# Performance work log

Hardware: AMD Instinct MI355X
Metric: run time of the kernel (lower is better)

## Reference

```python
import jax, jax.numpy as jnp
import numpy as np
import math

NUM_HEADS = 8

def setup_inputs() -> dict:
    key = jax.random.key(0)
    ks = jax.random.split(key, 5)
    b, h, w, c = 4, 128, 128, 256
    x = jax.random.normal(ks[0], (b, h, w, c), dtype=jnp.float32)
    scale = 1.0 / math.sqrt(c)  # keep weights reasonably scaled (kaiming-like)
    Wq = jax.random.normal(ks[1], (c, c), dtype=jnp.float32) * scale
    Wk = jax.random.normal(ks[2], (c, c), dtype=jnp.float32) * scale
    Wv = jax.random.normal(ks[3], (c, c), dtype=jnp.float32) * scale
    Wout = jax.random.normal(ks[4], (c, c), dtype=jnp.float32) * scale
    return {"x": x, "Wq": Wq, "Wk": Wk, "Wv": Wv, "Wout": Wout}

def reference(x, Wq, Wk, Wv, Wout):
    b, h, w, c = x.shape
    hw = h * w
    heads = NUM_HEADS
    dh = c // heads
    xs = x.reshape(b, hw, c)
    q = xs @ Wq  # (b, hw, c)
    k = xs @ Wk
    v = xs @ Wv

    def split_heads(t):
        # (b, hw, c) -> (b, c, hw) -> (b, heads, dh, hw)
        return t.transpose(0, 2, 1).reshape(b, heads, dh, hw)

    q = split_heads(q)
    k = split_heads(k)
    v = split_heads(v)
    # L2-normalize along the feature (hw) axis; original has no epsilon
    q = q / jnp.linalg.norm(q, axis=-1, keepdims=True)
    k = k / jnp.linalg.norm(k, axis=-1, keepdims=True)
    d_k = q.shape[-1]  # = hw
    attn = jnp.einsum('bhcd,bhed->bhce', q, k) / math.sqrt(d_k)  # (b,heads,dh,dh)
    attn = jax.nn.softmax(attn, axis=-1)
    vals = jnp.einsum('bhce,bhed->bhcd', attn, v)  # (b,heads,dh,hw)
    vals = vals.transpose(0, 3, 1, 2).reshape(b, hw, c)
    out = (vals @ Wout).reshape(b, h, w, c)
    return out
```

## Files before the change

### kernel.cpp

```cpp
#include <hip/hip_runtime.h>


#define B_   4
#define HW_  16384
#define C_   256

typedef __attribute__((ext_vector_type(8))) short short8;
typedef __attribute__((ext_vector_type(4))) float floatx4;

__device__ __forceinline__ unsigned short f2bf(float f) {
  unsigned u = __builtin_bit_cast(unsigned, f);
  u += 0x7FFFu + ((u >> 16) & 1u);
  return (unsigned short)(u >> 16);
}

__device__ __forceinline__ void gl_lds16(const unsigned short* g, unsigned short* l) {
  __builtin_amdgcn_global_load_lds(
      (const __attribute__((address_space(1))) unsigned int*)g,
      (__attribute__((address_space(3))) unsigned int*)l, 16, 0, 0);
}

__global__ __launch_bounds__(256) void k_cast_tr(const float* __restrict__ x,
                                                 unsigned short* __restrict__ xb,
                                                 unsigned short* __restrict__ xT,
                                                 float* __restrict__ S) {
  __shared__ unsigned short lds[64][72];
  int bid = blockIdx.x;
  int t = threadIdx.x;
  if (bid < 256) {
    float4 z = {0.f, 0.f, 0.f, 0.f};
    ((float4*)S)[bid * 256 + t] = z;
  }
  int ct = bid & 3;
  int pt = (bid >> 2) & 255;
  int b  = bid >> 10;
  const float* src = x + ((size_t)(b * HW_ + pt * 64)) * C_ + ct * 64;
#pragma unroll
  for (int e = 0; e < 4; e++) {
    int lin = t + e * 256;
    int p = lin >> 4, c4 = lin & 15;
    float4 v = *(const float4*)(src + (size_t)p * C_ + c4 * 4);
    ushort4 h;
    h.x = f2bf(v.x); h.y = f2bf(v.y); h.z = f2bf(v.z); h.w = f2bf(v.w);
    *(ushort4*)(xb + ((size_t)(b * HW_ + pt * 64 + p)) * C_ + ct * 64 + c4 * 4) = h;
    lds[c4 * 4 + 0][p] = h.x;
    lds[c4 * 4 + 1][p] = h.y;
    lds[c4 * 4 + 2][p] = h.z;
    lds[c4 * 4 + 3][p] = h.w;
  }
  __syncthreads();
#pragma unroll
  for (int e = 0; e < 4; e++) {
    int lin = t + e * 256;
    int c = lin >> 4, p4 = lin & 15;
    ushort4 h;
    h.x = lds[c][p4 * 4 + 0];
    h.y = lds[c][p4 * 4 + 1];
    h.z = lds[c][p4 * 4 + 2];
    h.w = lds[c][p4 * 4 + 3];
    *(ushort4*)(xT + ((size_t)(b * C_ + ct * 64 + c)) * HW_ + pt * 64 + p4 * 4) = h;
  }
}

template <int NST>
__device__ __forceinline__ void nt_loop(const unsigned short* Ab, int lda,
                                        const unsigned short* Bb, int ldb,
                                        unsigned short* At, unsigned short* Bt,
                                        floatx4 acc[4][4]) {
  int t = threadIdx.x;
  int lane = t & 63, w = t >> 6;
  int wm = w >> 1, wn = w & 1;
  int l8 = lane >> 3, l7 = lane & 7;
  int srcoct = l7 ^ l8;
  int l15 = lane & 15, l4 = lane >> 4;
  for (int s = 0; s < NST; s++) {
#pragma unroll
    for (int i = 0; i < 4; i++) {
      int gi = w * 4 + i;
      int row = gi * 8 + l8;
      gl_lds16(Ab + (size_t)row * lda + s * 64 + srcoct * 8, At + gi * 512);
      gl_lds16(Bb + (size_t)row * ldb + s * 64 + srcoct * 8, Bt + gi * 512);
    }
    __syncthreads();
#pragma unroll
    for (int kk = 0; kk < 2; kk++) {
      short8 af[4], bfv[4];
#pragma unroll
      for (int tm = 0; tm < 4; tm++) {
        int row = wm * 64 + tm * 16 + l15;
        int oct = kk * 4 + l4;
        af[tm] = *(const short8*)(At + row * 64 + ((oct ^ (l15 & 7)) * 8));
      }
#pragma unroll
      for (int tn = 0; tn < 4; tn++) {
        int row = wn * 64 + tn * 16 + l15;
        int oct = kk * 4 + l4;
        bfv[tn] = *(const short8*)(Bt + row * 64 + ((oct ^ (l15 & 7)) * 8));
      }
#pragma unroll
      for (int tm = 0; tm < 4; tm++)
#pragma unroll
        for (int tn = 0; tn < 4; tn++)
          acc[tm][tn] = __builtin_amdgcn_mfma_f32_16x16x32_bf16(af[tm], bfv[tn],
                                                                acc[tm][tn], 0, 0, 0);
    }
    __syncthreads();
  }
}

__global__ __launch_bounds__(256) void k_sgemm(const unsigned short* __restrict__ xT,
                                               float* __restrict__ S) {
  __shared__ unsigned short At[128 * 64];
  __shared__ unsigned short Bt[128 * 64];
  int bid = blockIdx.x;
  int ks = bid & 31, nt = (bid >> 5) & 1, mt = (bid >> 6) & 1, b = bid >> 7;
  const unsigned short* Ab = xT + ((size_t)(b * C_ + mt * 128)) * HW_ + ks * 512;
  const unsigned short* Bb = xT + ((size_t)(b * C_ + nt * 128)) * HW_ + ks * 512;
  floatx4 acc[4][4];
  floatx4 z = {0.f, 0.f, 0.f, 0.f};
#pragma unroll
  for (int i = 0; i < 4; i++)
#pragma unroll
    for (int j = 0; j < 4; j++) acc[i][j] = z;
  nt_loop<8>(Ab, HW_, Bb, HW_, At, Bt, acc);
  int t = threadIdx.x, lane = t & 63, w = t >> 6;
  int wm = w >> 1, wn = w & 1;
  int l15 = lane & 15, l4 = lane >> 4;
  float* Sb = S + (size_t)b * 65536;
#pragma unroll
  for (int tm = 0; tm < 4; tm++)
#pragma unroll
    for (int tn = 0; tn < 4; tn++)
#pragma unroll
      for (int r = 0; r < 4; r++) {
        int m = mt * 128 + wm * 64 + tm * 16 + l4 * 4 + r;
        int n = nt * 128 + wn * 64 + tn * 16 + l15;
        atomicAdd(Sb + (size_t)m * C_ + n, acc[tm][tn][r]);
      }
}

__global__ __launch_bounds__(256) void k_gemm_sw(const float* __restrict__ S,
                                                 const float* __restrict__ Wq,
                                                 const float* __restrict__ Wk,
                                                 float* __restrict__ SWq,
                                                 float* __restrict__ SWk) {
  __shared__ float As[64][17];
  __shared__ float Bs[16][65];
  int bid = blockIdx.x;
  int nt = bid & 7, mt = (bid >> 3) & 3, b = bid >> 5;
  int mb = mt * 64;
  const float* Wsel = (nt < 4) ? Wq : Wk;
  int nb = (nt & 3) * 64;
  int t = threadIdx.x, tx = t & 15, ty = t >> 4;
  float acc[4][4] = {};
  for (int kt = 0; kt < 16; kt++) {
    {
      int row = t >> 2, kq = t & 3;
      float4 v = *(const float4*)(S + ((size_t)(b * C_ + mb + row)) * C_ + kt * 16 + kq * 4);
      As[row][kq * 4 + 0] = v.x; As[row][kq * 4 + 1] = v.y;
      As[row][kq * 4 + 2] = v.z; As[row][kq * 4 + 3] = v.w;
    }
    {
      int kk = t >> 4, n4 = t & 15;
      float4 v = *(const float4*)(Wsel + ((size_t)(kt * 16 + kk)) * C_ + nb + n4 * 4);
      Bs[kk][n4 * 4 + 0] = v.x; Bs[kk][n4 * 4 + 1] = v.y;
      Bs[kk][n4 * 4 + 2] = v.z; Bs[kk][n4 * 4 + 3] = v.w;
    }
    __syncthreads();
#pragma unroll
    for (int k = 0; k < 16; k++) {
      float a[4], bb[4];
#pragma unroll
      for (int i = 0; i < 4; i++) a[i] = As[ty * 4 + i][k];
#pragma unroll
      for (int j = 0; j < 4; j++) bb[j] = Bs[k][tx * 4 + j];
#pragma unroll
      for (int i = 0; i < 4; i++)
#pragma unroll
        for (int j = 0; j < 4; j++) acc[i][j] += a[i] * bb[j];
    }
    __syncthreads();
  }
#pragma unroll
  for (int i = 0; i < 4; i++)
#pragma unroll
    for (int j = 0; j < 4; j++) {
      int row = mb + ty * 4 + i;
      int ng = nt * 64 + tx * 4 + j;
      if (ng < 256) SWq[((size_t)(b * C_ + row)) * C_ + ng] = acc[i][j];
      else          SWk[((size_t)(b * C_ + row)) * C_ + ng - 256] = acc[i][j];
    }
}

__global__ __launch_bounds__(256) void k_fuse(const float* __restrict__ Wq,
                                              const float* __restrict__ Wk,
                                              const float* __restrict__ SWq,
                                              const float* __restrict__ SWk,
                                              const float* __restrict__ Wout,
                                              float* __restrict__ U) {
  __shared__ float Wqh[256][32];
  __shared__ float Wkh[256][32];
  __shared__ float SWqh[256][32];
  __shared__ float SWkh[256][32];
  __shared__ float Lg[32][33];
  __shared__ float qp[8][32], kp[8][32], qin[32], kin[32];
  int b = blockIdx.x >> 3, h = blockIdx.x & 7;
  int t = threadIdx.x;
  int col = t & 31, rgrp = t >> 5;
  for (int r0 = 0; r0 < 256; r0 += 8) {
    int row = r0 + rgrp;
    Wqh[row][col]  = Wq[(size_t)row * C_ + h * 32 + col];
    Wkh[row][col]  = Wk[(size_t)row * C_ + h * 32 + col];
    SWqh[row][col] = SWq[((size_t)(b * C_ + row)) * C_ + h * 32 + col];
    SWkh[row][col] = SWk[((size_t)(b * C_ + row)) * C_ + h * 32 + col];
  }
  __syncthreads();
  {
    float g[4] = {0.f, 0.f, 0.f, 0.f};
    for (int k = 0; k < 256; k++) {
      float swk = SWkh[k][col];
#pragma unroll
      for (int r = 0; r < 4; r++) g[r] += Wqh[k][rgrp + 8 * r] * swk;
    }
#pragma unroll
    for (int r = 0; r < 4; r++) Lg[rgrp + 8 * r][col] = g[r];
  }
  {
    float sq = 0.f, sk = 0.f;
    for (int k = rgrp * 32; k < rgrp * 32 + 32; k++) {
      sq += Wqh[k][col] * SWqh[k][col];
      sk += Wkh[k][col] * SWkh[k][col];
    }
    qp[rgrp][col] = sq;
    kp[rgrp][col] = sk;
  }
  __syncthreads();
  if (t < 32) {
    float a = 0.f;
#pragma unroll
    for (int p = 0; p < 8; p++) a += qp[p][t];
    qin[t] = rsqrtf(a);
  } else if (t < 64) {
    int j = t - 32;
    float a = 0.f;
#pragma unroll
    for (int p = 0; p < 8; p++) a += kp[p][j];
    kin[j] = rsqrtf(a);
  }
  __syncthreads();
  if (t < 32) {
    float row[32];
    float mx = -1e30f;
#pragma unroll
    for (int j = 0; j < 32; j++) {
      row[j] = Lg[t][j] * qin[t] * kin[j] * 0.0078125f;
      mx = fmaxf(mx, row[j]);
    }
    float sum = 0.f;
#pragma unroll
    for (int j = 0; j < 32; j++) { row[j] = __expf(row[j] - mx); sum += row[j]; }
    float inv = 1.0f / sum;
#pragma unroll
    for (int j = 0; j < 32; j++) Lg[t][j] = row[j] * inv;
  }
  __syncthreads();
  float (*Wo)[256] = reinterpret_cast<float(*)[256]>(&Wqh[0][0]);
#pragma unroll
  for (int r = 0; r < 32; r++) Wo[r][t] = Wout[((size_t)(h * 32 + r)) * C_ + t];
  __syncthreads();
  for (int j = 0; j < 32; j++) {
    float a = 0.f;
#pragma unroll
    for (int i2 = 0; i2 < 32; i2++) a += Lg[i2][j] * Wo[i2][t];
    U[((size_t)(b * C_ + h * 32 + j)) * C_ + t] = a;
  }
}

__global__ __launch_bounds__(256) void k_gemm_w3(const float* __restrict__ Wv,
                                                 const float* __restrict__ U,
                                                 unsigned short* __restrict__ W3bT) {
  __shared__ float As[64][17];
  __shared__ float Bs[16][65];
  int bid = blockIdx.x;
  int nt = bid & 3, mt = (bid >> 2) & 3, b = bid >> 4;
  int mb = mt * 64, nb = nt * 64;
  int t = threadIdx.x, tx = t & 15, ty = t >> 4;
  float acc[4][4] = {};
  for (int kt = 0; kt < 16; kt++) {
    {
      int row = t >> 2, kq = t & 3;
      float4 v = *(const float4*)(Wv + ((size_t)(mb + row)) * C_ + kt * 16 + kq * 4);
      As[row][kq * 4 + 0] = v.x; As[row][kq * 4 + 1] = v.y;
      As[row][kq * 4 + 2] = v.z; As[row][kq * 4 + 3] = v.w;
    }
    {
      int kk = t >> 4, n4 = t & 15;
      float4 v = *(const float4*)(U + ((size_t)(b * C_ + kt * 16 + kk)) * C_ + nb + n4 * 4);
      Bs[kk][n4 * 4 + 0] = v.x; Bs[kk][n4 * 4 + 1] = v.y;
      Bs[kk][n4 * 4 + 2] = v.z; Bs[kk][n4 * 4 + 3] = v.w;
    }
    __syncthreads();
#pragma unroll
    for (int k = 0; k < 16; k++) {
      float a[4], bb[4];
#pragma unroll
      for (int i = 0; i < 4; i++) a[i] = As[ty * 4 + i][k];
#pragma unroll
      for (int j = 0; j < 4; j++) bb[j] = Bs[k][tx * 4 + j];
#pragma unroll
      for (int i = 0; i < 4; i++)
#pragma unroll
        for (int j = 0; j < 4; j++) acc[i][j] += a[i] * bb[j];
    }
    __syncthreads();
  }
#pragma unroll
  for (int i = 0; i < 4; i++)
#pragma unroll
    for (int j = 0; j < 4; j++)
      W3bT[((size_t)(b * C_ + nb + tx * 4 + j)) * C_ + mb + ty * 4 + i] = f2bf(acc[i][j]);
}

__global__ __launch_bounds__(256) void k_out(const unsigned short* __restrict__ xb,
                                             const unsigned short* __restrict__ W3bT,
                                             float* __restrict__ out) {
  __shared__ unsigned short At[128 * 64];
  __shared__ unsigned short Bt[128 * 64];
  int bid = blockIdx.x;
  int ntile = bid & 1, mtile = bid >> 1;
  int b = mtile >> 7;
  const unsigned short* Ab = xb + (size_t)mtile * 128 * C_;
  const unsigned short* Bb = W3bT + ((size_t)(b * C_ + ntile * 128)) * C_;
  floatx4 acc[4][4];
  floatx4 z = {0.f, 0.f, 0.f, 0.f};
#pragma unroll
  for (int i = 0; i < 4; i++)
#pragma unroll
    for (int j = 0; j < 4; j++) acc[i][j] = z;
  nt_loop<4>(Ab, C_, Bb, C_, At, Bt, acc);
  int t = threadIdx.x, lane = t & 63, w = t >> 6;
  int wm = w >> 1, wn = w & 1;
  int l15 = lane & 15, l4 = lane >> 4;
  float* ob = out + (size_t)mtile * 128 * C_ + ntile * 128;
#pragma unroll
  for (int tm = 0; tm < 4; tm++)
#pragma unroll
    for (int tn = 0; tn < 4; tn++)
#pragma unroll
      for (int r = 0; r < 4; r++) {
        int m = wm * 64 + tm * 16 + l4 * 4 + r;
        int n = wn * 64 + tn * 16 + l15;
        ob[(size_t)m * C_ + n] = acc[tm][tn][r];
      }
}

extern "C" void kernel_launch(void* const* d_in, const int* in_sizes, int n_in,
                              void* d_out, int out_size, void* d_ws, size_t ws_size,
                              hipStream_t stream) {
  const float* x    = (const float*)d_in[0];
  const float* Wq   = (const float*)d_in[1];
  const float* Wk   = (const float*)d_in[2];
  const float* Wv   = (const float*)d_in[3];
  const float* Wout = (const float*)d_in[4];
  float* out = (float*)d_out;

  unsigned short* xT = (unsigned short*)d_ws;
  unsigned short* xb = xT + (size_t)16777216;
  float* S    = (float*)(xb + (size_t)16777216);
  float* SWq  = S + 262144;
  float* SWk  = SWq + 262144;
  float* U    = SWk + 262144;
  unsigned short* W3bT = (unsigned short*)(U + 262144);

  k_cast_tr<<<dim3(4096), dim3(256), 0, stream>>>(x, xb, xT, S);
  k_sgemm<<<dim3(512), dim3(256), 0, stream>>>(xT, S);
  k_gemm_sw<<<dim3(128), dim3(256), 0, stream>>>(S, Wq, Wk, SWq, SWk);
  k_fuse<<<dim3(32), dim3(256), 0, stream>>>(Wq, Wk, SWq, SWk, Wout, U);
  k_gemm_w3<<<dim3(64), dim3(256), 0, stream>>>(Wv, U, W3bT);
  k_out<<<dim3(1024), dim3(256), 0, stream>>>(xb, W3bT, out);
}
```

Baseline: 240.5 us.

## Replace atomic split-K reduction with partial buffers and a separate reduce kernel

The Gram-matrix GEMM now writes each split-K block's partial tile to its own buffer, and a new reduction kernel sums the 32 partials into S. This replaces the per-element float atomics and removes the zero-initialisation of S from the cast kernel. The GEMM also stages 256-wide K chunks in two phases with a wider XOR swizzle, so it needs fewer barriers. In exchange it adds a 32 MB partial buffer write and read, an extra kernel launch, and 128 KB of LDS per block, which limits occupancy to one block per CU.

```diff
diff --git a/kernel.cpp b/kernel.cpp
--- a/kernel.cpp
+++ b/kernel.cpp
@@ -22,15 +22,10 @@
 
 __global__ __launch_bounds__(256) void k_cast_tr(const float* __restrict__ x,
                                                  unsigned short* __restrict__ xb,
-                                                 unsigned short* __restrict__ xT,
-                                                 float* __restrict__ S) {
+                                                 unsigned short* __restrict__ xT) {
   __shared__ unsigned short lds[64][72];
   int bid = blockIdx.x;
   int t = threadIdx.x;
-  if (bid < 256) {
-    float4 z = {0.f, 0.f, 0.f, 0.f};
-    ((float4*)S)[bid * 256 + t] = z;
-  }
   int ct = bid & 3;
   int pt = (bid >> 2) & 255;
   int b  = bid >> 10;
@@ -62,81 +57,83 @@
   }
 }
 
-template <int NST>
-__device__ __forceinline__ void nt_loop(const unsigned short* Ab, int lda,
-                                        const unsigned short* Bb, int ldb,
-                                        unsigned short* At, unsigned short* Bt,
-                                        floatx4 acc[4][4]) {
-  int t = threadIdx.x;
-  int lane = t & 63, w = t >> 6;
-  int wm = w >> 1, wn = w & 1;
-  int l8 = lane >> 3, l7 = lane & 7;
-  int srcoct = l7 ^ l8;
-  int l15 = lane & 15, l4 = lane >> 4;
-  for (int s = 0; s < NST; s++) {
-#pragma unroll
-    for (int i = 0; i < 4; i++) {
-      int gi = w * 4 + i;
-      int row = gi * 8 + l8;
-      gl_lds16(Ab + (size_t)row * lda + s * 64 + srcoct * 8, At + gi * 512);
-      gl_lds16(Bb + (size_t)row * ldb + s * 64 + srcoct * 8, Bt + gi * 512);
-    }
-    __syncthreads();
-#pragma unroll
-    for (int kk = 0; kk < 2; kk++) {
-      short8 af[4], bfv[4];
-#pragma unroll
-      for (int tm = 0; tm < 4; tm++) {
-        int row = wm * 64 + tm * 16 + l15;
-        int oct = kk * 4 + l4;
-        af[tm] = *(const short8*)(At + row * 64 + ((oct ^ (l15 & 7)) * 8));
-      }
-#pragma unroll
-      for (int tn = 0; tn < 4; tn++) {
-        int row = wn * 64 + tn * 16 + l15;
-        int oct = kk * 4 + l4;
-        bfv[tn] = *(const short8*)(Bt + row * 64 + ((oct ^ (l15 & 7)) * 8));
-      }
-#pragma unroll
-      for (int tm = 0; tm < 4; tm++)
-#pragma unroll
-        for (int tn = 0; tn < 4; tn++)
-          acc[tm][tn] = __builtin_amdgcn_mfma_f32_16x16x32_bf16(af[tm], bfv[tn],
-                                                                acc[tm][tn], 0, 0, 0);
-    }
-    __syncthreads();
-  }
-}
-
 __global__ __launch_bounds__(256) void k_sgemm(const unsigned short* __restrict__ xT,
-                                               float* __restrict__ S) {
-  __shared__ unsigned short At[128 * 64];
-  __shared__ unsigned short Bt[128 * 64];
+                                               float* __restrict__ part) {
+  __shared__ unsigned short At[128 * 256];
+  __shared__ unsigned short Bt[128 * 256];
   int bid = blockIdx.x;
   int ks = bid & 31, nt = (bid >> 5) & 1, mt = (bid >> 6) & 1, b = bid >> 7;
   const unsigned short* Ab = xT + ((size_t)(b * C_ + mt * 128)) * HW_ + ks * 512;
   const unsigned short* Bb = xT + ((size_t)(b * C_ + nt * 128)) * HW_ + ks * 512;
-  floatx4 acc[4][4];
-  floatx4 z = {0.f, 0.f, 0.f, 0.f};
-#pragma unroll
-  for (int i = 0; i < 4; i++)
-#pragma unroll
-    for (int j = 0; j < 4; j++) acc[i][j] = z;
-  nt_loop<8>(Ab, HW_, Bb, HW_, At, Bt, acc);
   int t = threadIdx.x, lane = t & 63, w = t >> 6;
   int wm = w >> 1, wn = w & 1;
   int l15 = lane & 15, l4 = lane >> 4;
-  float* Sb = S + (size_t)b * 65536;
+  int lrow = lane >> 5;
+  int lslot = lane & 31;
+  floatx4 acc[4][4];
+  floatx4 z = {0.f, 0.f, 0.f, 0.f};
+#pragma unroll
+  for (int i = 0; i < 4; i++)
+#pragma unroll
+    for (int j = 0; j < 4; j++) acc[i][j] = z;
+
+  for (int ph = 0; ph < 2; ph++) {
+    if (ph) __syncthreads();
+#pragma unroll
+    for (int i = 0; i < 16; i++) {
+      int issue = w * 16 + i;
+      int row = issue * 2 + lrow;
+      int goct = lslot ^ (row & 31);
+      gl_lds16(Ab + (size_t)row * HW_ + ph * 256 + goct * 8, At + issue * 512);
+      gl_lds16(Bb + (size_t)row * HW_ + ph * 256 + goct * 8, Bt + issue * 512);
+    }
+    __syncthreads();
+#pragma unroll
+    for (int kk = 0; kk < 8; kk++) {
+      short8 af[4], bfv[4];
+      int oct = kk * 4 + l4;
+#pragma unroll
+      for (int tm = 0; tm < 4; tm++) {
+        int row = wm * 64 + tm * 16 + l15;
+        af[tm] = *(const short8*)(At + row * 256 + ((oct ^ (row & 31)) * 8));
+      }
+#pragma unroll
+      for (int tn = 0; tn < 4; tn++) {
+        int row = wn * 64 + tn * 16 + l15;
+        bfv[tn] = *(const short8*)(Bt + row * 256 + ((oct ^ (row & 31)) * 8));
+      }
+#pragma unroll
+      for (int tm = 0; tm < 4; tm++)
+#pragma unroll
+        for (int tn = 0; tn < 4; tn++)
+          acc[tm][tn] = __builtin_amdgcn_mfma_f32_16x16x32_bf16(af[tm], bfv[tn],
+                                                                acc[tm][tn], 0, 0, 0);
+    }
+  }
+  float* pb = part + (size_t)bid * 16384;
 #pragma unroll
   for (int tm = 0; tm < 4; tm++)
 #pragma unroll
     for (int tn = 0; tn < 4; tn++)
 #pragma unroll
       for (int r = 0; r < 4; r++) {
-        int m = mt * 128 + wm * 64 + tm * 16 + l4 * 4 + r;
-        int n = nt * 128 + wn * 64 + tn * 16 + l15;
-        atomicAdd(Sb + (size_t)m * C_ + n, acc[tm][tn][r]);
-      }
+        int m = wm * 64 + tm * 16 + l4 * 4 + r;
+        int n = wn * 64 + tn * 16 + l15;
+        pb[m * 128 + n] = acc[tm][tn][r];
+      }
+}
+
+__global__ __launch_bounds__(256) void k_sred(const float* __restrict__ part,
+                                              float* __restrict__ S) {
+  int idx = blockIdx.x * 256 + threadIdx.x;
+  int b = idx >> 16;
+  int m = (idx >> 8) & 255, n = idx & 255;
+  const float* p = part + ((size_t)((b * 4 + (m >> 7) * 2 + (n >> 7)) * 32)) * 16384
+                   + (m & 127) * 128 + (n & 127);
+  float s = 0.f;
+#pragma unroll
+  for (int k = 0; k < 32; k++) s += p[k * 16384];
+  S[idx] = s;
 }
 
 __global__ __launch_bounds__(256) void k_gemm_sw(const float* __restrict__ S,
@@ -331,16 +328,50 @@
   int b = mtile >> 7;
   const unsigned short* Ab = xb + (size_t)mtile * 128 * C_;
   const unsigned short* Bb = W3bT + ((size_t)(b * C_ + ntile * 128)) * C_;
+  int t = threadIdx.x, lane = t & 63, w = t >> 6;
+  int wm = w >> 1, wn = w & 1;
+  int l8 = lane >> 3, l7 = lane & 7;
+  int srcoct = l7 ^ l8;
+  int l15 = lane & 15, l4 = lane >> 4;
   floatx4 acc[4][4];
   floatx4 z = {0.f, 0.f, 0.f, 0.f};
 #pragma unroll
   for (int i = 0; i < 4; i++)
 #pragma unroll
     for (int j = 0; j < 4; j++) acc[i][j] = z;
-  nt_loop<4>(Ab, C_, Bb, C_, At, Bt, acc);
-  int t = threadIdx.x, lane = t & 63, w = t >> 6;
-  int wm = w >> 1, wn = w & 1;
-  int l15 = lane & 15, l4 = lane >> 4;
+  for (int s = 0; s < 4; s++) {
+    if (s) __syncthreads();
+#pragma unroll
+    for (int i = 0; i < 4; i++) {
+      int gi = w * 4 + i;
+      int row = gi * 8 + l8;
+      gl_lds16(Ab + (size_t)row * C_ + s * 64 + srcoct * 8, At + gi * 512);
+      gl_lds16(Bb + (size_t)row * C_ + s * 64 + srcoct * 8, Bt + gi * 512);
+    }
+    __syncthreads();
+#pragma unroll
+    for (int kk = 0; kk < 2; kk++) {
+      short8 af[4], bfv[4];
+#pragma unroll
+      for (int tm = 0; tm < 4; tm++) {
+        int row = wm * 64 + tm * 16 + l15;
+        int oct = kk * 4 + l4;
+        af[tm] = *(const short8*)(At + row * 64 + ((oct ^ (l15 & 7)) * 8));
+      }
+#pragma unroll
+      for (int tn = 0; tn < 4; tn++) {
+        int row = wn * 64 + tn * 16 + l15;
+        int oct = kk * 4 + l4;
+        bfv[tn] = *(const short8*)(Bt + row * 64 + ((oct ^ (l15 & 7)) * 8));
+      }
+#pragma unroll
+      for (int tm = 0; tm < 4; tm++)
+#pragma unroll
+        for (int tn = 0; tn < 4; tn++)
+          acc[tm][tn] = __builtin_amdgcn_mfma_f32_16x16x32_bf16(af[tm], bfv[tn],
+                                                                acc[tm][tn], 0, 0, 0);
+    }
+  }
   float* ob = out + (size_t)mtile * 128 * C_ + ntile * 128;
 #pragma unroll
   for (int tm = 0; tm < 4; tm++)
@@ -366,14 +397,16 @@
 
   unsigned short* xT = (unsigned short*)d_ws;
   unsigned short* xb = xT + (size_t)16777216;
-  float* S    = (float*)(xb + (size_t)16777216);
+  float* part = (float*)(xb + (size_t)16777216);
+  float* S    = part + (size_t)8388608;
   float* SWq  = S + 262144;
   float* SWk  = SWq + 262144;
   float* U    = SWk + 262144;
   unsigned short* W3bT = (unsigned short*)(U + 262144);
 
-  k_cast_tr<<<dim3(4096), dim3(256), 0, stream>>>(x, xb, xT, S);
-  k_sgemm<<<dim3(512), dim3(256), 0, stream>>>(xT, S);
+  k_cast_tr<<<dim3(4096), dim3(256), 0, stream>>>(x, xb, xT);
+  k_sgemm<<<dim3(512), dim3(256), 0, stream>>>(xT, part);
+  k_sred<<<dim3(1024), dim3(256), 0, stream>>>(part, S);
   k_gemm_sw<<<dim3(128), dim3(256), 0, stream>>>(S, Wq, Wk, SWq, SWk);
   k_fuse<<<dim3(32), dim3(256), 0, stream>>>(Wq, Wk, SWq, SWk, Wout, U);
   k_gemm_w3<<<dim3(64), dim3(256), 0, stream>>>(Wv, U, W3bT);
```

Result: faster. 232.3 us (-3.4%).
